# Optimization experiments

Measured on AMD Instinct MI355X. Metric: run time of the kernel, lower is better.

Reference implementation:

```python
import jax, jax.numpy as jnp
import numpy as np

N, NODE_DIM, EDGE_DIM, E, H, L, G = 100000, 128, 16, 1200000, 64, 3, 1000


def gcn_conv(x, w, b, row, col, dis):
    # PyG GCNConv: x @ W, symmetric-normalized aggregation with self-loops, + bias
    xw = x @ w                                    # [N, H]
    norm = dis[row] * dis[col]                    # [E]
    msg = norm[:, None] * xw[row]                 # [E, H]
    out = jax.ops.segment_sum(msg, col, num_segments=N)
    out = out + (dis * dis)[:, None] * xw         # self-loop contribution
    return out + b


def reference(x, edge_attr, node_w, node_b, edge_w, edge_b, conv_w, conv_b,
              cls_w1, cls_b1, cls_w2, cls_b2, edge_index, batch, num_graphs):
    row, col = edge_index[0], edge_index[1]
    # node embed
    h = x @ node_w + node_b                       # [N, H]
    # edge embed aggregated to both endpoints
    e = edge_attr @ edge_w + edge_b               # [E, H]
    edge_aggr = jax.ops.segment_sum(e, row, num_segments=N) \
              + jax.ops.segment_sum(e, col, num_segments=N)
    h = h + edge_aggr
    # degree with self-loops (deg over col, matching PyG GCNConv default flow)
    deg = jax.ops.segment_sum(jnp.ones((E,), h.dtype), col, num_segments=N) + 1.0
    dis = jnp.where(deg > 0, jax.lax.rsqrt(deg), 0.0)
    xs = []
    for i in range(L):
        h = jax.nn.relu(gcn_conv(h, conv_w[i], conv_b[i], row, col, dis))
        xs.append(h)
    hj = jnp.concatenate(xs, axis=-1)             # JumpingKnowledge 'cat' -> [N, L*H]
    # global mean pool over batch index
    sums = jax.ops.segment_sum(hj, batch, num_segments=num_graphs)
    cnts = jax.ops.segment_sum(jnp.ones((N,), hj.dtype), batch, num_segments=num_graphs)
    pooled = sums / jnp.maximum(cnts, 1.0)[:, None]  # [G, L*H]
    # classifier (eval mode: dropout is identity)
    z = jax.nn.relu(pooled @ cls_w1 + cls_b1)
    out = z @ cls_w2 + cls_b2                     # [G, 1]
    return out.squeeze(-1)


def setup_inputs() -> dict:
    key = jax.random.key(0)
    ks = jax.random.split(key, 16)
    s = lambda fan: 1.0 / np.sqrt(fan)
    return {
        "x": jax.random.normal(ks[0], (N, NODE_DIM), jnp.float32),
        "edge_attr": jax.random.normal(ks[1], (E, EDGE_DIM), jnp.float32),
        "node_w": jax.random.uniform(ks[2], (NODE_DIM, H), jnp.float32, -s(NODE_DIM), s(NODE_DIM)),
        "node_b": jnp.zeros((H,), jnp.float32),
        "edge_w": jax.random.uniform(ks[3], (EDGE_DIM, H), jnp.float32, -s(EDGE_DIM), s(EDGE_DIM)),
        "edge_b": jnp.zeros((H,), jnp.float32),
        "conv_w": jax.random.uniform(ks[4], (L, H, H), jnp.float32, -s(H), s(H)),
        "conv_b": jnp.zeros((L, H), jnp.float32),
        "cls_w1": jax.random.uniform(ks[5], (L * H, H // 2), jnp.float32, -s(L * H), s(L * H)),
        "cls_b1": jnp.zeros((H // 2,), jnp.float32),
        "cls_w2": jax.random.uniform(ks[6], (H // 2, 1), jnp.float32, -s(H // 2), s(H // 2)),
        "cls_b2": jnp.zeros((1,), jnp.float32),
        "edge_index": jax.random.randint(ks[7], (2, E), 0, N, jnp.int64 if jax.config.jax_enable_x64 else jnp.int32),
        "batch": jnp.sort(jax.random.randint(ks[8], (N,), 0, G, jnp.int64 if jax.config.jax_enable_x64 else jnp.int32)),
        "num_graphs": G,
    }
```

## Files before the change

### kernel.cpp

```cpp
#include <hip/hip_runtime.h>
#include <math.h>


#define EPB 4096

__global__ __launch_bounds__(256) void k_embed(
    const float* __restrict__ x, const float* __restrict__ w,
    const float* __restrict__ b, float* __restrict__ out, int N) {
  __shared__ __align__(16) float rl[64 * 128];
  const int t = threadIdx.x;
  const int j = t & 63;
  const int wv = t >> 6;
  const int base = blockIdx.x * 64;
  float wr[128];
#pragma unroll
  for (int k = 0; k < 128; ++k) wr[k] = w[k * 64 + j];
  const float bj = b[j];
#pragma unroll
  for (int it = 0; it < 8; ++it) {
    int lin = (t + it * 256) * 4;
    int r = lin >> 7, c = lin & 127;
    int row = base + r;
    float4 v = (row < N) ? *(const float4*)&x[(size_t)row * 128 + c]
                         : make_float4(0.f, 0.f, 0.f, 0.f);
    *(float4*)&rl[lin] = v;
  }
  __syncthreads();
  for (int r = wv; r < 64; r += 4) {
    int row = base + r;
    if (row >= N) break;
    float acc = bj;
#pragma unroll
    for (int k4 = 0; k4 < 32; ++k4) {
      float4 a = *(const float4*)&rl[r * 128 + k4 * 4];
      acc = fmaf(a.x, wr[k4 * 4 + 0], acc);
      acc = fmaf(a.y, wr[k4 * 4 + 1], acc);
      acc = fmaf(a.z, wr[k4 * 4 + 2], acc);
      acc = fmaf(a.w, wr[k4 * 4 + 3], acc);
    }
    out[(size_t)row * 64 + j] = acc;
  }
}

__global__ __launch_bounds__(256) void k_conv(
    const float* __restrict__ hin, const float* __restrict__ w,
    const float* __restrict__ dis, float* __restrict__ xws, int N) {
  __shared__ __align__(16) float rl[64 * 64];
  const int t = threadIdx.x;
  const int j = t & 63;
  const int wv = t >> 6;
  const int base = blockIdx.x * 64;
  float wr[64];
#pragma unroll
  for (int k = 0; k < 64; ++k) wr[k] = w[k * 64 + j];
#pragma unroll
  for (int it = 0; it < 4; ++it) {
    int lin = (t + it * 256) * 4;
    int r = lin >> 6, c = lin & 63;
    int row = base + r;
    float4 v = (row < N) ? *(const float4*)&hin[(size_t)row * 64 + c]
                         : make_float4(0.f, 0.f, 0.f, 0.f);
    *(float4*)&rl[lin] = v;
  }
  __syncthreads();
  for (int r = wv; r < 64; r += 4) {
    int row = base + r;
    if (row >= N) break;
    float acc = 0.f;
#pragma unroll
    for (int k4 = 0; k4 < 16; ++k4) {
      float4 a = *(const float4*)&rl[r * 64 + k4 * 4];
      acc = fmaf(a.x, wr[k4 * 4 + 0], acc);
      acc = fmaf(a.y, wr[k4 * 4 + 1], acc);
      acc = fmaf(a.z, wr[k4 * 4 + 2], acc);
      acc = fmaf(a.w, wr[k4 * 4 + 3], acc);
    }
    xws[(size_t)row * 64 + j] = dis[row] * acc;
  }
}

__global__ __launch_bounds__(256) void k_hist(
    const int* __restrict__ erow, const int* __restrict__ ecol,
    int* __restrict__ matTc, int* __restrict__ matTr, int E, int NB, int NBLK) {
  __shared__ int hc[512], hr[512];
  int b = blockIdx.x, t = threadIdx.x;
  for (int i = t; i < NB; i += 256) { hc[i] = 0; hr[i] = 0; }
  __syncthreads();
  int e0 = b * EPB;
#pragma unroll
  for (int q = 0; q < 16; ++q) {
    int e = e0 + q * 256 + t;
    if (e < E) {
      atomicAdd(&hc[ecol[e] >> 8], 1);
      atomicAdd(&hr[erow[e] >> 8], 1);
    }
  }
  __syncthreads();
  for (int i = t; i < NB; i += 256) {
    matTc[(size_t)i * NBLK + b] = hc[i];
    matTr[(size_t)i * NBLK + b] = hr[i];
  }
}

__global__ __launch_bounds__(256) void kBscan(
    int* __restrict__ matT, int* __restrict__ tot, int NBLK) {
  __shared__ int sc[256];
  int i = blockIdx.x, t = threadIdx.x;
  int* row = matT + (size_t)i * NBLK;
  int e0 = (2 * t < NBLK) ? row[2 * t] : 0;
  int e1 = (2 * t + 1 < NBLK) ? row[2 * t + 1] : 0;
  int s = e0 + e1;
  sc[t] = s;
  __syncthreads();
  for (int d = 1; d < 256; d <<= 1) {
    int x = (t >= d) ? sc[t - d] : 0;
    __syncthreads();
    sc[t] += x;
    __syncthreads();
  }
  int excl = sc[t] - s;
  if (2 * t < NBLK) row[2 * t] = excl;
  if (2 * t + 1 < NBLK) row[2 * t + 1] = excl + e0;
  if (t == 255) tot[i] = sc[255];
}

__global__ __launch_bounds__(512) void kB2(
    const int* __restrict__ tot, int* __restrict__ start, int NB) {
  __shared__ int sc[512];
  int t = threadIdx.x;
  int s = (t < NB) ? tot[t] : 0;
  sc[t] = s;
  __syncthreads();
  for (int d = 1; d < 512; d <<= 1) {
    int x = (t >= d) ? sc[t - d] : 0;
    __syncthreads();
    sc[t] += x;
    __syncthreads();
  }
  if (t < NB) start[t] = sc[t] - s;
}

__global__ __launch_bounds__(256) void k_scat(
    const int* __restrict__ erow, const int* __restrict__ ecol,
    const int* __restrict__ matTc, const int* __restrict__ matTr,
    const int* __restrict__ startc, const int* __restrict__ startr,
    unsigned long long* __restrict__ tmpc, unsigned int* __restrict__ tmpr,
    int E, int NB, int NBLK) {
  __shared__ int curc[512], curr[512];
  int b = blockIdx.x, t = threadIdx.x;
  for (int i = t; i < NB; i += 256) {
    curc[i] = startc[i] + matTc[(size_t)i * NBLK + b];
    curr[i] = startr[i] + matTr[(size_t)i * NBLK + b];
  }
  __syncthreads();
  int e0 = b * EPB;
#pragma unroll
  for (int q = 0; q < 16; ++q) {
    int e = e0 + q * 256 + t;
    if (e < E) {
      int r = erow[e], c = ecol[e];
      int pc = atomicAdd(&curc[c >> 8], 1);
      tmpc[pc] = (unsigned long long)(c & 255) |
                 ((unsigned long long)r << 8) |
                 ((unsigned long long)e << 25);
      int pr = atomicAdd(&curr[r >> 8], 1);
      tmpr[pr] = ((unsigned int)e << 8) | (unsigned int)(r & 255);
    }
  }
}

__global__ __launch_bounds__(256) void k_bcount_c(
    const unsigned long long* __restrict__ tmpc, const int* __restrict__ startc,
    const int* __restrict__ totc, int* __restrict__ indeg,
    int* __restrict__ offc, int N) {
  __shared__ int h[256], sc[256];
  int b = blockIdx.x, t = threadIdx.x;
  h[t] = 0;
  __syncthreads();
  int bstart = startc[b], cnt = totc[b];
  for (int i = t; i < cnt; i += 256)
    atomicAdd(&h[(int)(tmpc[bstart + i] & 255)], 1);
  __syncthreads();
  int s = h[t];
  sc[t] = s;
  __syncthreads();
  for (int d = 1; d < 256; d <<= 1) {
    int x = (t >= d) ? sc[t - d] : 0;
    __syncthreads();
    sc[t] += x;
    __syncthreads();
  }
  int n = (b << 8) + t;
  if (n < N) {
    indeg[n] = s;
    offc[n] = bstart + sc[t] - s;
  }
}

__global__ __launch_bounds__(256) void k_bcount_r(
    const unsigned int* __restrict__ tmpr, const int* __restrict__ startr,
    const int* __restrict__ totr, int* __restrict__ outdeg,
    int* __restrict__ offr, int N) {
  __shared__ int h[256], sc[256];
  int b = blockIdx.x, t = threadIdx.x;
  h[t] = 0;
  __syncthreads();
  int bstart = startr[b], cnt = totr[b];
  for (int i = t; i < cnt; i += 256)
    atomicAdd(&h[(int)(tmpr[bstart + i] & 255)], 1);
  __syncthreads();
  int s = h[t];
  sc[t] = s;
  __syncthreads();
  for (int d = 1; d < 256; d <<= 1) {
    int x = (t >= d) ? sc[t - d] : 0;
    __syncthreads();
    sc[t] += x;
    __syncthreads();
  }
  int n = (b << 8) + t;
  if (n < N) {
    outdeg[n] = s;
    offr[n] = bstart + sc[t] - s;
  }
}

__global__ __launch_bounds__(256) void k_place_c(
    const unsigned long long* __restrict__ tmpc, const int* __restrict__ offc,
    int2* __restrict__ lst2, int N, int E) {
  __shared__ int cur[256];
  int b = blockIdx.x, t = threadIdx.x;
  int colbase = b << 8;
  int nb = min(256, N - colbase);
  if (t < nb) cur[t] = offc[colbase + t];
  __syncthreads();
  int bstart = offc[colbase];
  int bend = (colbase + 256 < N) ? offc[colbase + 256] : E;
  for (int idx = bstart + t; idx < bend; idx += 256) {
    unsigned long long v = tmpc[idx];
    int lc = (int)(v & 255);
    int src = (int)((v >> 8) & 0x1FFFF);
    int eid = (int)(v >> 25);
    int p = atomicAdd(&cur[lc], 1);
    int2 w; w.x = src; w.y = eid;
    lst2[p] = w;
  }
}

__global__ __launch_bounds__(256) void k_place_r(
    const unsigned int* __restrict__ tmpr, const int* __restrict__ offr,
    int* __restrict__ eidr, int N, int E) {
  __shared__ int cur[256];
  int b = blockIdx.x, t = threadIdx.x;
  int rowbase = b << 8;
  int nb = min(256, N - rowbase);
  if (t < nb) cur[t] = offr[rowbase + t];
  __syncthreads();
  int bstart = offr[rowbase];
  int bend = (rowbase + 256 < N) ? offr[rowbase + 256] : E;
  for (int idx = bstart + t; idx < bend; idx += 256) {
    unsigned int v = tmpr[idx];
    int lr = (int)(v & 255);
    int p = atomicAdd(&cur[lr], 1);
    eidr[p] = (int)(v >> 8);
  }
}

__global__ __launch_bounds__(256) void k_eembed(
    const float* __restrict__ ea, const int2* __restrict__ lst2,
    const int* __restrict__ eidr, const int* __restrict__ offc,
    const int* __restrict__ indeg, const int* __restrict__ offr,
    const int* __restrict__ outdeg, const float* __restrict__ ew,
    const float* __restrict__ eb, float* h0, float* __restrict__ dis, int N) {
  int t = blockIdx.x * 256 + threadIdx.x;
  int n = __builtin_amdgcn_readfirstlane(t >> 6);
  if (n >= N) return;
  int lane = threadIdx.x & 63;
  int slot = lane >> 4, kk = lane & 15;
  int cin = indeg[n], basec = offc[n];
  int cout = outdeg[n], baser = offr[n];
  float acc = 0.f;
  int c0 = (cin > 0) ? cin - 1 : 0;
  for (int i = 0; i < cin; i += 16) {
#pragma unroll
    for (int q = 0; q < 4; ++q) {
      int idx = i + q * 4 + slot;
      int eid = lst2[basec + min(idx, c0)].y;
      float v = ea[(size_t)eid * 16 + kk];
      acc += (idx < cin) ? v : 0.f;
    }
  }
  int r0 = (cout > 0) ? cout - 1 : 0;
  for (int i = 0; i < cout; i += 16) {
#pragma unroll
    for (int q = 0; q < 4; ++q) {
      int idx = i + q * 4 + slot;
      int eid = eidr[baser + min(idx, r0)];
      float v = ea[(size_t)eid * 16 + kk];
      acc += (idx < cout) ? v : 0.f;
    }
  }
  acc += __shfl_xor(acc, 16, 64);
  acc += __shfl_xor(acc, 32, 64);
  int j = lane;
  float v = h0[(size_t)n * 64 + j] + (float)(cin + cout) * eb[j];
#pragma unroll
  for (int k = 0; k < 16; ++k) {
    float ak = __shfl(acc, k, 64);
    v = fmaf(ak, ew[k * 64 + j], v);
  }
  h0[(size_t)n * 64 + j] = v;
  if (j == 0) dis[n] = 1.0f / sqrtf((float)cin + 1.0f);
}

__global__ __launch_bounds__(256) void k_gather(
    const float* __restrict__ xws, const float* __restrict__ dis,
    const int* __restrict__ offc, const int* __restrict__ indeg,
    const int2* __restrict__ lst2, const float* __restrict__ b,
    float* __restrict__ h0, float* __restrict__ hj_slice, int N) {
  int t = blockIdx.x * 256 + threadIdx.x;
  int j = t & 63;
  int n = __builtin_amdgcn_readfirstlane(t >> 6);
  if (n >= N) return;
  int cnt = indeg[n];
  int base = offc[n];
  int c0 = (cnt > 0) ? cnt - 1 : 0;
  float acc = xws[(size_t)n * 64 + j];
  for (int i = 0; i < cnt; i += 16) {
    float s[16];
#pragma unroll
    for (int q = 0; q < 16; ++q) {
      int src = lst2[base + min(i + q, c0)].x;
      s[q] = xws[(size_t)src * 64 + j];
    }
#pragma unroll
    for (int q = 0; q < 16; ++q)
      acc += (i + q < cnt) ? s[q] : 0.f;
  }
  float act = fmaxf(fmaf(dis[n], acc, b[j]), 0.f);
  h0[(size_t)n * 64 + j] = act;
  hj_slice[(size_t)n * 192 + j] = act;
}

__global__ __launch_bounds__(192) void k_pool(
    const float* __restrict__ hj, const int* __restrict__ batch, int N,
    const float* __restrict__ w1, const float* __restrict__ b1,
    const float* __restrict__ w2, const float* __restrict__ b2,
    float* __restrict__ out) {
  __shared__ float pl[192];
  int g = blockIdx.x;
  int t = threadIdx.x;
  int lo = 0, hi = N;
  while (lo < hi) { int m = (lo + hi) >> 1; if (batch[m] < g) lo = m + 1; else hi = m; }
  int start = lo;
  hi = N;
  while (lo < hi) { int m = (lo + hi) >> 1; if (batch[m] < g + 1) lo = m + 1; else hi = m; }
  int end = lo;
  float s = 0.f;
  for (int r = start; r < end; ++r) s += hj[(size_t)r * 192 + t];
  int cnt = end - start;
  pl[t] = s / (float)(cnt > 0 ? cnt : 1);
  __syncthreads();
  if (t < 64) {
    float val = 0.f;
    if (t < 32) {
      float z = b1[t];
#pragma unroll 8
      for (int k = 0; k < 192; ++k) z = fmaf(pl[k], w1[k * 32 + t], z);
      z = fmaxf(z, 0.f);
      val = z * w2[t];
    }
#pragma unroll
    for (int off = 16; off > 0; off >>= 1) val += __shfl_down(val, off);
    if (t == 0) out[g] = val + b2[0];
  }
}

extern "C" void kernel_launch(void* const* d_in, const int* in_sizes, int n_in,
                              void* d_out, int out_size, void* d_ws, size_t ws_size,
                              hipStream_t stream) {
  const float* x      = (const float*)d_in[0];
  const float* ea     = (const float*)d_in[1];
  const float* node_w = (const float*)d_in[2];
  const float* node_b = (const float*)d_in[3];
  const float* edge_w = (const float*)d_in[4];
  const float* edge_b = (const float*)d_in[5];
  const float* conv_w = (const float*)d_in[6];
  const float* conv_b = (const float*)d_in[7];
  const float* w1     = (const float*)d_in[8];
  const float* b1     = (const float*)d_in[9];
  const float* w2     = (const float*)d_in[10];
  const float* b2     = (const float*)d_in[11];
  const int*   ei     = (const int*)d_in[12];
  const int*   batch  = (const int*)d_in[13];

  const int N = in_sizes[0] / 128;
  const int E = in_sizes[12] / 2;
  const int G = out_size;
  const int* erow = ei;
  const int* ecol = ei + E;

  float* ws = (float*)d_ws;
  size_t o = 0;
  float* h0    = ws + o; o += (size_t)N * 64;
  float* xws   = ws + o; o += (size_t)N * 64;
  float* hj    = ws + o; o += (size_t)N * 192;
  float* dis   = ws + o; o += N;
  int* indeg   = (int*)(ws + o); o += N;
  int* outdeg  = (int*)(ws + o); o += N;
  int* offc    = (int*)(ws + o); o += N;
  int* offr    = (int*)(ws + o); o += N;
  int2* lst2   = (int2*)(ws + o); o += (size_t)2 * E;

  const int NB = (N + 255) >> 8;
  const int NBLK = (E + EPB - 1) / EPB;
  unsigned long long* tmpc = (unsigned long long*)hj;
  unsigned int* tmpr = (unsigned int*)(hj + (size_t)2 * E);
  int* eidr  = (int*)(hj + (size_t)3 * E);
  int* matTc = (int*)(hj + (size_t)4 * E);
  int* matTr = matTc + (size_t)NB * NBLK;
  int* totc  = matTr + (size_t)NB * NBLK;
  int* startc = totc + NB;
  int* totr  = startc + NB;
  int* startr = totr + NB;
  float* out = (float*)d_out;

  dim3 b256(256);

  k_embed<<<(N + 63) / 64, b256, 0, stream>>>(x, node_w, node_b, h0, N);
  k_hist<<<NBLK, b256, 0, stream>>>(erow, ecol, matTc, matTr, E, NB, NBLK);
  kBscan<<<NB, b256, 0, stream>>>(matTc, totc, NBLK);
  kBscan<<<NB, b256, 0, stream>>>(matTr, totr, NBLK);
  kB2<<<1, dim3(512), 0, stream>>>(totc, startc, NB);
  kB2<<<1, dim3(512), 0, stream>>>(totr, startr, NB);
  k_scat<<<NBLK, b256, 0, stream>>>(erow, ecol, matTc, matTr, startc, startr,
                                    tmpc, tmpr, E, NB, NBLK);
  k_bcount_c<<<NB, b256, 0, stream>>>(tmpc, startc, totc, indeg, offc, N);
  k_bcount_r<<<NB, b256, 0, stream>>>(tmpr, startr, totr, outdeg, offr, N);
  k_place_c<<<NB, b256, 0, stream>>>(tmpc, offc, lst2, N, E);
  k_place_r<<<NB, b256, 0, stream>>>(tmpr, offr, eidr, N, E);
  k_eembed<<<((size_t)N * 64 + 255) / 256, b256, 0, stream>>>(
      ea, lst2, eidr, offc, indeg, offr, outdeg, edge_w, edge_b, h0, dis, N);
  for (int l = 0; l < 3; ++l) {
    k_conv<<<(N + 63) / 64, b256, 0, stream>>>(
        h0, conv_w + (size_t)l * 64 * 64, dis, xws, N);
    k_gather<<<((size_t)N * 64 + 255) / 256, b256, 0, stream>>>(
        xws, dis, offc, indeg, lst2, conv_b + (size_t)l * 64,
        h0, hj + (size_t)l * 64, N);
  }
  k_pool<<<G, dim3(192), 0, stream>>>(hj, batch, N, w1, b1, w2, b2, out);
}
```

Measured before the change: 473.0 us.

## Fuse GCN dense transforms into edge-embed and gather kernels; split CSR arrays

```diff
diff --git a/kernel.cpp b/kernel.cpp
--- a/kernel.cpp
+++ b/kernel.cpp
@@ -39,43 +39,6 @@
       acc = fmaf(a.w, wr[k4 * 4 + 3], acc);
     }
     out[(size_t)row * 64 + j] = acc;
-  }
-}
-
-__global__ __launch_bounds__(256) void k_conv(
-    const float* __restrict__ hin, const float* __restrict__ w,
-    const float* __restrict__ dis, float* __restrict__ xws, int N) {
-  __shared__ __align__(16) float rl[64 * 64];
-  const int t = threadIdx.x;
-  const int j = t & 63;
-  const int wv = t >> 6;
-  const int base = blockIdx.x * 64;
-  float wr[64];
-#pragma unroll
-  for (int k = 0; k < 64; ++k) wr[k] = w[k * 64 + j];
-#pragma unroll
-  for (int it = 0; it < 4; ++it) {
-    int lin = (t + it * 256) * 4;
-    int r = lin >> 6, c = lin & 63;
-    int row = base + r;
-    float4 v = (row < N) ? *(const float4*)&hin[(size_t)row * 64 + c]
-                         : make_float4(0.f, 0.f, 0.f, 0.f);
-    *(float4*)&rl[lin] = v;
-  }
-  __syncthreads();
-  for (int r = wv; r < 64; r += 4) {
-    int row = base + r;
-    if (row >= N) break;
-    float acc = 0.f;
-#pragma unroll
-    for (int k4 = 0; k4 < 16; ++k4) {
-      float4 a = *(const float4*)&rl[r * 64 + k4 * 4];
-      acc = fmaf(a.x, wr[k4 * 4 + 0], acc);
-      acc = fmaf(a.y, wr[k4 * 4 + 1], acc);
-      acc = fmaf(a.z, wr[k4 * 4 + 2], acc);
-      acc = fmaf(a.w, wr[k4 * 4 + 3], acc);
-    }
-    xws[(size_t)row * 64 + j] = dis[row] * acc;
   }
 }
 
@@ -227,7 +190,7 @@
 
 __global__ __launch_bounds__(256) void k_place_c(
     const unsigned long long* __restrict__ tmpc, const int* __restrict__ offc,
-    int2* __restrict__ lst2, int N, int E) {
+    int* __restrict__ srcl, int* __restrict__ eidc, int N, int E) {
   __shared__ int cur[256];
   int b = blockIdx.x, t = threadIdx.x;
   int colbase = b << 8;
@@ -242,8 +205,8 @@
     int src = (int)((v >> 8) & 0x1FFFF);
     int eid = (int)(v >> 25);
     int p = atomicAdd(&cur[lc], 1);
-    int2 w; w.x = src; w.y = eid;
-    lst2[p] = w;
+    srcl[p] = src;
+    eidc[p] = eid;
   }
 }
 
@@ -266,80 +229,141 @@
   }
 }
 
-__global__ __launch_bounds__(256) void k_eembed(
-    const float* __restrict__ ea, const int2* __restrict__ lst2,
-    const int* __restrict__ eidr, const int* __restrict__ offc,
-    const int* __restrict__ indeg, const int* __restrict__ offr,
-    const int* __restrict__ outdeg, const float* __restrict__ ew,
-    const float* __restrict__ eb, float* h0, float* __restrict__ dis, int N) {
-  int t = blockIdx.x * 256 + threadIdx.x;
-  int n = __builtin_amdgcn_readfirstlane(t >> 6);
-  if (n >= N) return;
-  int lane = threadIdx.x & 63;
-  int slot = lane >> 4, kk = lane & 15;
-  int cin = indeg[n], basec = offc[n];
-  int cout = outdeg[n], baser = offr[n];
-  float acc = 0.f;
-  int c0 = (cin > 0) ? cin - 1 : 0;
-  for (int i = 0; i < cin; i += 16) {
-#pragma unroll
-    for (int q = 0; q < 4; ++q) {
-      int idx = i + q * 4 + slot;
-      int eid = lst2[basec + min(idx, c0)].y;
-      float v = ea[(size_t)eid * 16 + kk];
-      acc += (idx < cin) ? v : 0.f;
-    }
-  }
-  int r0 = (cout > 0) ? cout - 1 : 0;
-  for (int i = 0; i < cout; i += 16) {
-#pragma unroll
-    for (int q = 0; q < 4; ++q) {
-      int idx = i + q * 4 + slot;
-      int eid = eidr[baser + min(idx, r0)];
-      float v = ea[(size_t)eid * 16 + kk];
-      acc += (idx < cout) ? v : 0.f;
-    }
-  }
-  acc += __shfl_xor(acc, 16, 64);
-  acc += __shfl_xor(acc, 32, 64);
-  int j = lane;
-  float v = h0[(size_t)n * 64 + j] + (float)(cin + cout) * eb[j];
-#pragma unroll
-  for (int k = 0; k < 16; ++k) {
-    float ak = __shfl(acc, k, 64);
-    v = fmaf(ak, ew[k * 64 + j], v);
-  }
-  h0[(size_t)n * 64 + j] = v;
-  if (j == 0) dis[n] = 1.0f / sqrtf((float)cin + 1.0f);
-}
-
-__global__ __launch_bounds__(256) void k_gather(
-    const float* __restrict__ xws, const float* __restrict__ dis,
+__global__ __launch_bounds__(256) void k_eefc(
+    const float* __restrict__ e0, const float* __restrict__ ea,
+    const int* __restrict__ eidc, const int* __restrict__ eidr,
     const int* __restrict__ offc, const int* __restrict__ indeg,
-    const int2* __restrict__ lst2, const float* __restrict__ b,
-    float* __restrict__ h0, float* __restrict__ hj_slice, int N) {
-  int t = blockIdx.x * 256 + threadIdx.x;
-  int j = t & 63;
-  int n = __builtin_amdgcn_readfirstlane(t >> 6);
-  if (n >= N) return;
-  int cnt = indeg[n];
-  int base = offc[n];
-  int c0 = (cnt > 0) ? cnt - 1 : 0;
-  float acc = xws[(size_t)n * 64 + j];
-  for (int i = 0; i < cnt; i += 16) {
-    float s[16];
-#pragma unroll
-    for (int q = 0; q < 16; ++q) {
-      int src = lst2[base + min(i + q, c0)].x;
-      s[q] = xws[(size_t)src * 64 + j];
-    }
-#pragma unroll
-    for (int q = 0; q < 16; ++q)
-      acc += (i + q < cnt) ? s[q] : 0.f;
-  }
-  float act = fmaxf(fmaf(dis[n], acc, b[j]), 0.f);
-  h0[(size_t)n * 64 + j] = act;
-  hj_slice[(size_t)n * 192 + j] = act;
+    const int* __restrict__ offr, const int* __restrict__ outdeg,
+    const float* __restrict__ ew, const float* __restrict__ eb,
+    const float* __restrict__ w0, float* __restrict__ dis,
+    float* __restrict__ xws0, int N) {
+  __shared__ __align__(16) float hrow[64][64];
+  __shared__ float disl[64];
+  const int t = threadIdx.x;
+  const int lane = t & 63;
+  const int wv = t >> 6;
+  const int base = blockIdx.x * 64;
+  const int slot = lane >> 4, kk = lane & 15;
+  float ewr[16];
+#pragma unroll
+  for (int k = 0; k < 16; ++k) ewr[k] = ew[k * 64 + lane];
+  const float ebl = eb[lane];
+  for (int r = wv; r < 64; r += 4) {
+    int n = base + r;
+    float v = 0.f, d = 0.f;
+    if (n < N) {
+      int cin = indeg[n], basec = offc[n];
+      int cout = outdeg[n], baser = offr[n];
+      float acc = 0.f;
+      int c0 = (cin > 0) ? cin - 1 : 0;
+      for (int i = 0; i < cin; i += 16) {
+#pragma unroll
+        for (int q = 0; q < 4; ++q) {
+          int idx = i + q * 4 + slot;
+          int eid = eidc[basec + min(idx, c0)];
+          float u = ea[(size_t)eid * 16 + kk];
+          acc += (idx < cin) ? u : 0.f;
+        }
+      }
+      int r0 = (cout > 0) ? cout - 1 : 0;
+      for (int i = 0; i < cout; i += 16) {
+#pragma unroll
+        for (int q = 0; q < 4; ++q) {
+          int idx = i + q * 4 + slot;
+          int eid = eidr[baser + min(idx, r0)];
+          float u = ea[(size_t)eid * 16 + kk];
+          acc += (idx < cout) ? u : 0.f;
+        }
+      }
+      acc += __shfl_xor(acc, 16, 64);
+      acc += __shfl_xor(acc, 32, 64);
+      v = e0[(size_t)n * 64 + lane] + (float)(cin + cout) * ebl;
+#pragma unroll
+      for (int k = 0; k < 16; ++k)
+        v = fmaf(__shfl(acc, k, 64), ewr[k], v);
+      d = 1.0f / sqrtf((float)cin + 1.0f);
+      if (lane == 0) dis[n] = d;
+    }
+    hrow[r][lane] = v;
+    if (lane == 0) disl[r] = d;
+  }
+  __syncthreads();
+  float wr[64];
+#pragma unroll
+  for (int k = 0; k < 64; ++k) wr[k] = w0[k * 64 + lane];
+  for (int r = wv; r < 64; r += 4) {
+    int n = base + r;
+    if (n >= N) break;
+    float acc = 0.f;
+#pragma unroll
+    for (int k4 = 0; k4 < 16; ++k4) {
+      float4 a = *(const float4*)&hrow[r][k4 * 4];
+      acc = fmaf(a.x, wr[k4 * 4 + 0], acc);
+      acc = fmaf(a.y, wr[k4 * 4 + 1], acc);
+      acc = fmaf(a.z, wr[k4 * 4 + 2], acc);
+      acc = fmaf(a.w, wr[k4 * 4 + 3], acc);
+    }
+    xws0[(size_t)n * 64 + lane] = disl[r] * acc;
+  }
+}
+
+__global__ __launch_bounds__(256) void k_fgc(
+    const float* __restrict__ xin, const float* __restrict__ dis,
+    const int* __restrict__ offc, const int* __restrict__ indeg,
+    const int* __restrict__ srcl, const float* __restrict__ bprev,
+    const float* __restrict__ wnext, float* __restrict__ hj_slice,
+    float* __restrict__ xout, int N) {
+  __shared__ __align__(16) float arow[64][64];
+  __shared__ float disl[64];
+  const int t = threadIdx.x;
+  const int lane = t & 63;
+  const int wv = t >> 6;
+  const int base = blockIdx.x * 64;
+  const float bl = bprev[lane];
+  for (int r = wv; r < 64; r += 4) {
+    int n = base + r;
+    float act = 0.f, d = 0.f;
+    if (n < N) {
+      int cnt = indeg[n], boff = offc[n];
+      int c0 = (cnt > 0) ? cnt - 1 : 0;
+      float acc = xin[(size_t)n * 64 + lane];
+      for (int i = 0; i < cnt; i += 16) {
+        float s[16];
+#pragma unroll
+        for (int q = 0; q < 16; ++q) {
+          int src = srcl[boff + min(i + q, c0)];
+          s[q] = xin[(size_t)src * 64 + lane];
+        }
+#pragma unroll
+        for (int q = 0; q < 16; ++q)
+          acc += (i + q < cnt) ? s[q] : 0.f;
+      }
+      d = dis[n];
+      act = fmaxf(fmaf(d, acc, bl), 0.f);
+      hj_slice[(size_t)n * 192 + lane] = act;
+    }
+    arow[r][lane] = act;
+    if (lane == 0) disl[r] = d;
+  }
+  if (wnext == nullptr) return;
+  __syncthreads();
+  float wr[64];
+#pragma unroll
+  for (int k = 0; k < 64; ++k) wr[k] = wnext[k * 64 + lane];
+  for (int r = wv; r < 64; r += 4) {
+    int n = base + r;
+    if (n >= N) break;
+    float acc = 0.f;
+#pragma unroll
+    for (int k4 = 0; k4 < 16; ++k4) {
+      float4 a = *(const float4*)&arow[r][k4 * 4];
+      acc = fmaf(a.x, wr[k4 * 4 + 0], acc);
+      acc = fmaf(a.y, wr[k4 * 4 + 1], acc);
+      acc = fmaf(a.z, wr[k4 * 4 + 2], acc);
+      acc = fmaf(a.w, wr[k4 * 4 + 3], acc);
+    }
+    xout[(size_t)n * 64 + lane] = disl[r] * acc;
+  }
 }
 
 __global__ __launch_bounds__(192) void k_pool(
@@ -402,32 +426,35 @@
 
   float* ws = (float*)d_ws;
   size_t o = 0;
-  float* h0    = ws + o; o += (size_t)N * 64;
-  float* xws   = ws + o; o += (size_t)N * 64;
+  float* xwsA  = ws + o; o += (size_t)N * 64;
+  float* xwsB  = ws + o; o += (size_t)N * 64;
   float* hj    = ws + o; o += (size_t)N * 192;
   float* dis   = ws + o; o += N;
   int* indeg   = (int*)(ws + o); o += N;
   int* outdeg  = (int*)(ws + o); o += N;
   int* offc    = (int*)(ws + o); o += N;
   int* offr    = (int*)(ws + o); o += N;
-  int2* lst2   = (int2*)(ws + o); o += (size_t)2 * E;
+  int* srcl    = (int*)(ws + o); o += E;
+  int* eidc    = (int*)(ws + o); o += E;
+  int* eidr    = (int*)(ws + o); o += E;
 
   const int NB = (N + 255) >> 8;
   const int NBLK = (E + EPB - 1) / EPB;
   unsigned long long* tmpc = (unsigned long long*)hj;
   unsigned int* tmpr = (unsigned int*)(hj + (size_t)2 * E);
-  int* eidr  = (int*)(hj + (size_t)3 * E);
-  int* matTc = (int*)(hj + (size_t)4 * E);
+  int* matTc = (int*)(hj + (size_t)3 * E);
   int* matTr = matTc + (size_t)NB * NBLK;
   int* totc  = matTr + (size_t)NB * NBLK;
   int* startc = totc + NB;
   int* totr  = startc + NB;
   int* startr = totr + NB;
+  float* e0 = xwsB;
   float* out = (float*)d_out;
 
   dim3 b256(256);
-
-  k_embed<<<(N + 63) / 64, b256, 0, stream>>>(x, node_w, node_b, h0, N);
+  const int NT = (N + 63) / 64;
+
+  k_embed<<<NT, b256, 0, stream>>>(x, node_w, node_b, e0, N);
   k_hist<<<NBLK, b256, 0, stream>>>(erow, ecol, matTc, matTr, E, NB, NBLK);
   kBscan<<<NB, b256, 0, stream>>>(matTc, totc, NBLK);
   kBscan<<<NB, b256, 0, stream>>>(matTr, totr, NBLK);
@@ -437,16 +464,15 @@
                                     tmpc, tmpr, E, NB, NBLK);
   k_bcount_c<<<NB, b256, 0, stream>>>(tmpc, startc, totc, indeg, offc, N);
   k_bcount_r<<<NB, b256, 0, stream>>>(tmpr, startr, totr, outdeg, offr, N);
-  k_place_c<<<NB, b256, 0, stream>>>(tmpc, offc, lst2, N, E);
+  k_place_c<<<NB, b256, 0, stream>>>(tmpc, offc, srcl, eidc, N, E);
   k_place_r<<<NB, b256, 0, stream>>>(tmpr, offr, eidr, N, E);
-  k_eembed<<<((size_t)N * 64 + 255) / 256, b256, 0, stream>>>(
-      ea, lst2, eidr, offc, indeg, offr, outdeg, edge_w, edge_b, h0, dis, N);
-  for (int l = 0; l < 3; ++l) {
-    k_conv<<<(N + 63) / 64, b256, 0, stream>>>(
-        h0, conv_w + (size_t)l * 64 * 64, dis, xws, N);
-    k_gather<<<((size_t)N * 64 + 255) / 256, b256, 0, stream>>>(
-        xws, dis, offc, indeg, lst2, conv_b + (size_t)l * 64,
-        h0, hj + (size_t)l * 64, N);
-  }
+  k_eefc<<<NT, b256, 0, stream>>>(e0, ea, eidc, eidr, offc, indeg, offr, outdeg,
+                                  edge_w, edge_b, conv_w, dis, xwsA, N);
+  k_fgc<<<NT, b256, 0, stream>>>(xwsA, dis, offc, indeg, srcl, conv_b,
+                                 conv_w + (size_t)1 * 64 * 64, hj, xwsB, N);
+  k_fgc<<<NT, b256, 0, stream>>>(xwsB, dis, offc, indeg, srcl, conv_b + 64,
+                                 conv_w + (size_t)2 * 64 * 64, hj + 64, xwsA, N);
+  k_fgc<<<NT, b256, 0, stream>>>(xwsA, dis, offc, indeg, srcl, conv_b + 128,
+                                 nullptr, hj + 128, nullptr, N);
   k_pool<<<G, dim3(192), 0, stream>>>(hj, batch, N, w1, b1, w2, b2, out);
 }
```

Result: slower. 536.6 us (+13.5%).
